# Performance work log

Measured on AMD Instinct MI355X. Metric: run time of the kernel, lower is better.

## Reference

```python
import jax, jax.numpy as jnp
import numpy as np

B, S, D, H, F = 2, 2048, 1024, 16, 4096
DH = D // H
EPS = 1e-6


def setup_inputs() -> dict:
    key = jax.random.key(0)
    ks = jax.random.split(key, 8)
    x = jax.random.normal(ks[0], (B, S, D), dtype=jnp.float32)
    # causal mask, broadcastable over [B,H,S,S]
    attention_mask = jnp.tril(jnp.ones((S, S), dtype=bool))[None, None]
    Wqkv = jax.random.normal(ks[1], (3 * D, D), dtype=jnp.float32) * (1.0 / np.sqrt(D))
    Wout = jax.random.normal(ks[2], (D, D), dtype=jnp.float32) * (1.0 / np.sqrt(D))
    W1 = jax.random.normal(ks[3], (F, D), dtype=jnp.float32) * (1.0 / np.sqrt(D))
    b1 = jnp.zeros((F,), dtype=jnp.float32)
    W2 = jax.random.normal(ks[4], (D, F), dtype=jnp.float32) * (1.0 / np.sqrt(F))
    b2 = jnp.zeros((D,), dtype=jnp.float32)
    gamma1 = jnp.ones((D,), dtype=jnp.float32)
    beta1 = jnp.zeros((D,), dtype=jnp.float32)
    gamma2 = jnp.ones((D,), dtype=jnp.float32)
    beta2 = jnp.zeros((D,), dtype=jnp.float32)
    return {"x": x, "attention_mask": attention_mask, "Wqkv": Wqkv, "Wout": Wout,
            "W1": W1, "b1": b1, "W2": W2, "b2": b2,
            "gamma1": gamma1, "beta1": beta1, "gamma2": gamma2, "beta2": beta2}


def layer_norm(x, gamma, beta):
    # Matches torch module: (x - mean) / (std + eps), std unbiased=False
    mean = jnp.mean(x, axis=-1, keepdims=True)
    std = jnp.sqrt(jnp.mean((x - mean) ** 2, axis=-1, keepdims=True))
    return gamma * ((x - mean) / (std + EPS)) + beta


def reference(x, attention_mask, Wqkv, Wout, W1, b1, W2, b2, gamma1, beta1, gamma2, beta2):
    # --- attention sub-block (Pre-LN) ---
    h = layer_norm(x, gamma1, beta1)
    qkv = h @ Wqkv.T                                   # [B,S,3D]
    qkv = qkv.reshape(B, S, 3, H, DH).transpose(2, 0, 3, 1, 4)  # [3,B,H,S,DH]
    q, k, v = qkv[0], qkv[1], qkv[2]
    scale = DH ** -0.5
    scores = jnp.einsum('bhqd,bhkd->bhqk', q, k) * scale
    scores = jnp.where(attention_mask, scores, -jnp.inf)
    attn = jax.nn.softmax(scores, axis=-1)
    out = jnp.einsum('bhqk,bhkd->bhqd', attn, v)       # [B,H,S,DH]
    out = out.transpose(0, 2, 1, 3).reshape(B, S, D)
    out = out @ Wout.T
    x = x + out                                        # dropout eval = identity
    # --- FFN sub-block (Pre-LN) ---
    h = layer_norm(x, gamma2, beta2)
    h = jax.nn.gelu(h @ W1.T + b1, approximate=False)  # torch GELU default = exact erf
    h = h @ W2.T + b2
    return x + h
```

## Files before the change

### kernel.cpp

```cpp
#include <hip/hip_runtime.h>
#include <hip/hip_bf16.h>
#include <math.h>


typedef __bf16 bf16;
typedef __bf16 bf16x4 __attribute__((ext_vector_type(4)));
typedef __bf16 bf16x8 __attribute__((ext_vector_type(8)));
typedef float f32x4 __attribute__((ext_vector_type(4)));

#define LOG2E 1.4426950408889634f
#define NSHIFT -17.312340489f

__device__ __forceinline__ f32x4 mfma16(bf16x8 a, bf16x8 b, f32x4 c) {
    return __builtin_amdgcn_mfma_f32_16x16x32_bf16(a, b, c, 0, 0, 0);
}
__device__ __forceinline__ void load16_lds(const bf16* g, bf16* l) {
    __builtin_amdgcn_global_load_lds(
        (__attribute__((address_space(1))) void*)g,
        (__attribute__((address_space(3))) void*)l, 16, 0, 0);
}

__global__ __launch_bounds__(256) void cvt4_kernel(const float* __restrict__ s0,
                                                   const float* __restrict__ s1,
                                                   const float* __restrict__ s2,
                                                   const float* __restrict__ s3,
                                                   bf16* __restrict__ dst) {
    const int blk = blockIdx.x;
    const float* s;
    int base;
    if (blk < 3072)      { s = s0; base = blk * 1024; }
    else if (blk < 4096) { s = s1; base = (blk - 3072) * 1024; }
    else if (blk < 8192) { s = s2; base = (blk - 4096) * 1024; }
    else                 { s = s3; base = (blk - 8192) * 1024; }
    const int t4 = threadIdx.x * 4;
    const float4 f = *(const float4*)(s + base + t4);
    bf16x4 o;
    o[0] = (bf16)f.x; o[1] = (bf16)f.y; o[2] = (bf16)f.z; o[3] = (bf16)f.w;
    *(bf16x4*)(dst + (size_t)blk * 1024 + t4) = o;
}

__global__ __launch_bounds__(256) void ln_kernel(const float* __restrict__ xin,
                                                 bf16* __restrict__ out,
                                                 const float* __restrict__ gamma,
                                                 const float* __restrict__ beta) {
    const int row = blockIdx.x;
    const int tid = threadIdx.x;
    const float4 f = *(const float4*)(xin + (size_t)row * 1024 + tid * 4);
    float v[4] = {f.x, f.y, f.z, f.w};
    float s = v[0] + v[1] + v[2] + v[3];
    float s2 = v[0] * v[0] + v[1] * v[1] + v[2] * v[2] + v[3] * v[3];
#pragma unroll
    for (int off = 1; off < 64; off <<= 1) {
        s += __shfl_xor(s, off);
        s2 += __shfl_xor(s2, off);
    }
    __shared__ float red[8];
    const int wave = tid >> 6, lane = tid & 63;
    if (lane == 0) { red[wave] = s; red[4 + wave] = s2; }
    __syncthreads();
    s = red[0] + red[1] + red[2] + red[3];
    s2 = red[4] + red[5] + red[6] + red[7];
    const float mean = s * (1.0f / 1024.0f);
    float var = s2 * (1.0f / 1024.0f) - mean * mean;
    var = fmaxf(var, 0.0f);
    const float rstd = 1.0f / (sqrtf(var) + 1e-6f);
    const int c = tid * 4;
    const float4 g = *(const float4*)(gamma + c);
    const float4 b = *(const float4*)(beta + c);
    bf16x4 o;
    o[0] = (bf16)((v[0] - mean) * rstd * g.x + b.x);
    o[1] = (bf16)((v[1] - mean) * rstd * g.y + b.y);
    o[2] = (bf16)((v[2] - mean) * rstd * g.z + b.z);
    o[3] = (bf16)((v[3] - mean) * rstd * g.w + b.w);
    *(bf16x4*)(out + (size_t)row * 1024 + c) = o;
}

template <int EPI>
__global__ __launch_bounds__(256, 3) void gemm_bt(const bf16* __restrict__ A,
                                                  const bf16* __restrict__ B,
                                                  int N, int K, int ldk,
                                                  bf16* __restrict__ outb,
                                                  float* __restrict__ outf,
                                                  const float* __restrict__ bias,
                                                  const float* __restrict__ resf,
                                                  bf16* __restrict__ qk,
                                                  bf16* __restrict__ vt) {
    __shared__ alignas(16) bf16 As[2][128 * 32];
    __shared__ alignas(16) bf16 Bs[2][128 * 32];
    const int tid = threadIdx.x;
    const int bm = blockIdx.x, bn = blockIdx.y;
    const int wave = tid >> 6, lane = tid & 63;
    const int wm = (wave >> 1) * 64, wn = (wave & 1) * 64;
    const int l16 = lane & 15, quad = lane >> 4;

    f32x4 acc[4][4] = {};

    const size_t koff = (size_t)blockIdx.z * K;
    const int row0 = tid >> 2, ch0 = tid & 3;
    const int gch = ch0 ^ ((row0 >> 1) & 3);
    const bf16* Ap = A + (size_t)(bm * 128 + row0) * ldk + koff + gch * 8;
    const bf16* Bp = B + (size_t)(bn * 128 + row0) * ldk + koff + gch * 8;
    const size_t rstep = (size_t)64 * ldk;

#pragma unroll
    for (int r = 0; r < 2; r++) {
        load16_lds(Ap + r * rstep, &As[0][tid * 8 + r * 2048]);
        load16_lds(Bp + r * rstep, &Bs[0][tid * 8 + r * 2048]);
    }
    __syncthreads();

    int buf = 0;
    for (int k0 = 0; k0 < K; k0 += 32, buf ^= 1) {
        if (k0 + 32 < K) {
#pragma unroll
            for (int r = 0; r < 2; r++) {
                load16_lds(Ap + r * rstep + k0 + 32, &As[buf ^ 1][tid * 8 + r * 2048]);
                load16_lds(Bp + r * rstep + k0 + 32, &Bs[buf ^ 1][tid * 8 + r * 2048]);
            }
        }
        bf16x8 af[4], bfr[4];
#pragma unroll
        for (int i = 0; i < 4; i++) {
            const int ra = wm + i * 16 + l16;
            af[i] = *(const bf16x8*)(&As[buf][ra * 32 + (quad ^ ((ra >> 1) & 3)) * 8]);
        }
#pragma unroll
        for (int j = 0; j < 4; j++) {
            const int rb = wn + j * 16 + l16;
            bfr[j] = *(const bf16x8*)(&Bs[buf][rb * 32 + (quad ^ ((rb >> 1) & 3)) * 8]);
        }
#pragma unroll
        for (int i = 0; i < 4; i++)
#pragma unroll
            for (int j = 0; j < 4; j++) acc[i][j] = mfma16(af[i], bfr[j], acc[i][j]);
        __syncthreads();
    }

#pragma unroll
    for (int i = 0; i < 4; i++) {
#pragma unroll
        for (int j = 0; j < 4; j++) {
            const int gr0 = bm * 128 + wm + i * 16 + quad * 4;
            const int gc = bn * 128 + wn + j * 16 + l16;
            float bv = 0.0f;
            if (EPI == 2) bv = bias[gc];
            if (EPI == 5 && bias && blockIdx.z == 0) bv = bias[gc];
            if (EPI == 4 && gc >= 2048) {
                const int n = gc - 2048;
                const int hh = n >> 6, dd = n & 63;
                const int bb = gr0 >> 11, ss = gr0 & 2047;
                bf16x4 pk;
#pragma unroll
                for (int r = 0; r < 4; r++) pk[r] = (bf16)acc[i][j][r];
                *(bf16x4*)(vt + ((size_t)((bb * 16 + hh) * 64 + dd)) * 2048 + ss) = pk;
            } else {
#pragma unroll
                for (int r = 0; r < 4; r++) {
                    const float v = acc[i][j][r];
                    const size_t idx = (size_t)(gr0 + r) * N + gc;
                    if (EPI == 0) {
                        outb[idx] = (bf16)v;
                    } else if (EPI == 1) {
                        outf[idx] = v + resf[idx];
                    } else if (EPI == 2) {
                        const float t = v + bv;
                        outb[idx] = (bf16)(0.5f * t * (1.0f + erff(t * 0.70710678118654752f)));
                    } else if (EPI == 5) {
                        atomicAdd(&outf[idx], v + bv);
                    } else {
                        qk[(size_t)(gr0 + r) * 2048 + gc] = (bf16)v;
                    }
                }
            }
        }
    }
}

__global__ __launch_bounds__(256, 4) void flash_attn(const bf16* __restrict__ qk,
                                                     const bf16* __restrict__ vt,
                                                     bf16* __restrict__ attn) {
    __shared__ alignas(16) bf16 Ks[64 * 72];
    __shared__ alignas(16) bf16 Vs[64 * 72];
    __shared__ alignas(16) bf16 Ps[4][16 * 72];
    const int tid = threadIdx.x;
    const int wave = tid >> 6, lane = tid & 63;
    const int l16 = lane & 15, quad = lane >> 4;
    const int bh = blockIdx.x;
    const int qt = 31 - blockIdx.y;
    const int b = bh >> 4, h = bh & 15;
    const int q0w = qt * 64 + wave * 16;
    const bf16* qkb = qk + (size_t)b * 2048 * 2048;
    const bf16* vtb = vt + (size_t)bh * 64 * 2048;

    bf16x8 qf[2];
#pragma unroll
    for (int c = 0; c < 2; c++) {
        bf16x8 v = *(const bf16x8*)(qkb + (size_t)(q0w + l16) * 2048 +
                                    h * 64 + c * 32 + quad * 8);
#pragma unroll
        for (int e = 0; e < 8; e++) v[e] = (bf16)((float)v[e] * 0.125f);
        qf[c] = v;
    }

    float lsum[4] = {0.0f, 0.0f, 0.0f, 0.0f};
    f32x4 o[4] = {};

    const int ntiles = qt + 1;
    for (int t = 0; t < ntiles; t++) {
        const int k0 = t * 64;
#pragma unroll
        for (int i = 0; i < 2; i++) {
            const int r = i * 32 + (tid >> 3), ch = tid & 7;
            *(uint4*)(&Ks[r * 72 + ch * 8]) =
                *(const uint4*)(qkb + (size_t)(k0 + r) * 2048 + 1024 + h * 64 + ch * 8);
            *(uint4*)(&Vs[r * 72 + ch * 8]) =
                *(const uint4*)(vtb + (size_t)r * 2048 + k0 + ch * 8);
        }
        __syncthreads();
        f32x4 s[4];
#pragma unroll
        for (int kt = 0; kt < 4; kt++) {
            const bf16x8 k0f = *(const bf16x8*)(&Ks[(kt * 16 + l16) * 72 + quad * 8]);
            const bf16x8 k1f = *(const bf16x8*)(&Ks[(kt * 16 + l16) * 72 + 32 + quad * 8]);
            s[kt] = mfma16(qf[1], k1f, mfma16(qf[0], k0f, (f32x4){0, 0, 0, 0}));
        }
        const bool need_mask = (t == ntiles - 1);
#pragma unroll
        for (int r = 0; r < 4; r++) {
            const int qrow = q0w + quad * 4 + r;
            float e0 = exp2f(fmaf(s[0][r], LOG2E, NSHIFT));
            float e1 = exp2f(fmaf(s[1][r], LOG2E, NSHIFT));
            float e2 = exp2f(fmaf(s[2][r], LOG2E, NSHIFT));
            float e3 = exp2f(fmaf(s[3][r], LOG2E, NSHIFT));
            if (need_mask) {
                if (k0 + l16 > qrow) e0 = 0.0f;
                if (k0 + 16 + l16 > qrow) e1 = 0.0f;
                if (k0 + 32 + l16 > qrow) e2 = 0.0f;
                if (k0 + 48 + l16 > qrow) e3 = 0.0f;
            }
            lsum[r] += (e0 + e1) + (e2 + e3);
            bf16* pp = &Ps[wave][(quad * 4 + r) * 72];
            pp[l16] = (bf16)e0;
            pp[16 + l16] = (bf16)e1;
            pp[32 + l16] = (bf16)e2;
            pp[48 + l16] = (bf16)e3;
        }
#pragma unroll
        for (int c = 0; c < 2; c++) {
            const bf16x8 pf = *(const bf16x8*)(&Ps[wave][l16 * 72 + c * 32 + quad * 8]);
#pragma unroll
            for (int dt = 0; dt < 4; dt++) {
                const bf16x8 vf =
                    *(const bf16x8*)(&Vs[(dt * 16 + l16) * 72 + c * 32 + quad * 8]);
                o[dt] = mfma16(pf, vf, o[dt]);
            }
        }
        __syncthreads();
    }

#pragma unroll
    for (int r = 0; r < 4; r++) {
#pragma unroll
        for (int off = 1; off < 16; off <<= 1) lsum[r] += __shfl_xor(lsum[r], off);
        lsum[r] = 1.0f / fmaxf(lsum[r], 1e-30f);
    }
    bf16* ob = attn + (size_t)b * 2048 * 1024;
#pragma unroll
    for (int dt = 0; dt < 4; dt++)
#pragma unroll
        for (int r = 0; r < 4; r++) {
            const int q = q0w + quad * 4 + r;
            ob[(size_t)q * 1024 + h * 64 + dt * 16 + l16] = (bf16)(o[dt][r] * lsum[r]);
        }
}

extern "C" void kernel_launch(void* const* d_in, const int* in_sizes, int n_in,
                              void* d_out, int out_size, void* d_ws, size_t ws_size,
                              hipStream_t stream) {
    const float* x    = (const float*)d_in[0];
    const float* Wqkv = (const float*)d_in[2];
    const float* Wout = (const float*)d_in[3];
    const float* W1   = (const float*)d_in[4];
    const float* b1   = (const float*)d_in[5];
    const float* W2   = (const float*)d_in[6];
    const float* b2   = (const float*)d_in[7];
    const float* g1   = (const float*)d_in[8];
    const float* be1  = (const float*)d_in[9];
    const float* g2   = (const float*)d_in[10];
    const float* be2  = (const float*)d_in[11];

    char* ws = (char*)d_ws;
    bf16* Wb     = (bf16*)(ws);
    bf16* Wqkv_b = (bf16*)(ws);
    bf16* Wout_b = (bf16*)(ws + (6u << 20));
    bf16* W1_b   = (bf16*)(ws + (8u << 20));
    bf16* W2_b   = (bf16*)(ws + (16u << 20));
    bf16* h      = (bf16*)(ws + (24u << 20));
    bf16* qkbuf  = (bf16*)(ws + (32u << 20));
    bf16* vtbuf  = (bf16*)(ws + (48u << 20));
    bf16* attn   = (bf16*)(ws + (56u << 20));
    bf16* act    = (bf16*)(ws + (32u << 20));
    float* x2    = (float*)d_out;

    cvt4_kernel<<<12288, 256, 0, stream>>>(Wqkv, Wout, W1, W2, Wb);

    ln_kernel<<<4096, 256, 0, stream>>>(x, h, g1, be1);
    gemm_bt<4><<<dim3(32, 24), 256, 0, stream>>>(h, Wqkv_b, 3072, 1024, 1024,
                                                 nullptr, nullptr, nullptr, nullptr,
                                                 qkbuf, vtbuf);
    flash_attn<<<dim3(32, 32), 256, 0, stream>>>(qkbuf, vtbuf, attn);
    gemm_bt<1><<<dim3(32, 8), 256, 0, stream>>>(attn, Wout_b, 1024, 1024, 1024,
                                                nullptr, x2, nullptr, x, nullptr, nullptr);
    ln_kernel<<<4096, 256, 0, stream>>>(x2, h, g2, be2);
    gemm_bt<2><<<dim3(32, 32), 256, 0, stream>>>(h, W1_b, 4096, 1024, 1024,
                                                 act, nullptr, b1, nullptr, nullptr, nullptr);
    gemm_bt<5><<<dim3(32, 8, 2), 256, 0, stream>>>(act, W2_b, 1024, 2048, 4096,
                                                   nullptr, x2, b2, nullptr, nullptr, nullptr);
}
```

Before: 379.9 us.

## Add 256x256x64 GEMM kernel for QKV, FFN1 and split-K FFN2

Adds a 512-thread GEMM with 256x256 output tiles and a 64-wide K step, using an 8-chunk XOR swizzle in LDS. It replaces the 128x128 kernel for the QKV projection, FFN up-projection with GELU, and FFN down-projection, which now splits K four ways instead of two. Larger tiles raise arithmetic intensity and cut global traffic per FLOP. The cost is far fewer blocks (192/256 on a 256-CU part), 128KB LDS per block limiting occupancy, and more atomic adds in the down-projection.

```diff
diff --git a/kernel.cpp b/kernel.cpp
--- a/kernel.cpp
+++ b/kernel.cpp
@@ -82,9 +82,7 @@
                                                   bf16* __restrict__ outb,
                                                   float* __restrict__ outf,
                                                   const float* __restrict__ bias,
-                                                  const float* __restrict__ resf,
-                                                  bf16* __restrict__ qk,
-                                                  bf16* __restrict__ vt) {
+                                                  const float* __restrict__ resf) {
     __shared__ alignas(16) bf16 As[2][128 * 32];
     __shared__ alignas(16) bf16 Bs[2][128 * 32];
     const int tid = threadIdx.x;
@@ -95,11 +93,10 @@
 
     f32x4 acc[4][4] = {};
 
-    const size_t koff = (size_t)blockIdx.z * K;
     const int row0 = tid >> 2, ch0 = tid & 3;
     const int gch = ch0 ^ ((row0 >> 1) & 3);
-    const bf16* Ap = A + (size_t)(bm * 128 + row0) * ldk + koff + gch * 8;
-    const bf16* Bp = B + (size_t)(bn * 128 + row0) * ldk + koff + gch * 8;
+    const bf16* Ap = A + (size_t)(bm * 128 + row0) * ldk + gch * 8;
+    const bf16* Bp = B + (size_t)(bn * 128 + row0) * ldk + gch * 8;
     const size_t rstep = (size_t)64 * ldk;
 
 #pragma unroll
@@ -142,6 +139,94 @@
         for (int j = 0; j < 4; j++) {
             const int gr0 = bm * 128 + wm + i * 16 + quad * 4;
             const int gc = bn * 128 + wn + j * 16 + l16;
+#pragma unroll
+            for (int r = 0; r < 4; r++) {
+                const float v = acc[i][j][r];
+                const size_t idx = (size_t)(gr0 + r) * N + gc;
+                if (EPI == 1) {
+                    outf[idx] = v + resf[idx];
+                } else {
+                    outb[idx] = (bf16)v;
+                }
+            }
+        }
+    }
+}
+
+template <int EPI>
+__global__ __launch_bounds__(512, 2) void gemm256_bt(const bf16* __restrict__ A,
+                                                     const bf16* __restrict__ B,
+                                                     int N, int K, int ldk,
+                                                     bf16* __restrict__ outb,
+                                                     float* __restrict__ outf,
+                                                     const float* __restrict__ bias,
+                                                     bf16* __restrict__ qk,
+                                                     bf16* __restrict__ vt) {
+    __shared__ alignas(16) bf16 As[2][256 * 64];
+    __shared__ alignas(16) bf16 Bs[2][256 * 64];
+    const int tid = threadIdx.x;
+    const int bm = blockIdx.x, bn = blockIdx.y;
+    const int wave = tid >> 6, lane = tid & 63;
+    const int wm = (wave >> 2) * 128, wn = (wave & 3) * 64;
+    const int l16 = lane & 15, quad = lane >> 4;
+
+    f32x4 acc[8][4] = {};
+
+    const size_t koff = (size_t)blockIdx.z * K;
+    const int row0 = tid >> 3, ch0 = tid & 7;
+    const int gch = ch0 ^ (row0 & 7);
+    const bf16* Ap = A + (size_t)(bm * 256 + row0) * ldk + koff + gch * 8;
+    const bf16* Bp = B + (size_t)(bn * 256 + row0) * ldk + koff + gch * 8;
+    const size_t rstep = (size_t)64 * ldk;
+
+#pragma unroll
+    for (int r = 0; r < 4; r++) {
+        load16_lds(Ap + r * rstep, &As[0][(row0 + r * 64) * 64 + ch0 * 8]);
+        load16_lds(Bp + r * rstep, &Bs[0][(row0 + r * 64) * 64 + ch0 * 8]);
+    }
+    __syncthreads();
+
+    int buf = 0;
+    for (int k0 = 0; k0 < K; k0 += 64, buf ^= 1) {
+        if (k0 + 64 < K) {
+#pragma unroll
+            for (int r = 0; r < 4; r++) {
+                load16_lds(Ap + r * rstep + k0 + 64,
+                           &As[buf ^ 1][(row0 + r * 64) * 64 + ch0 * 8]);
+                load16_lds(Bp + r * rstep + k0 + 64,
+                           &Bs[buf ^ 1][(row0 + r * 64) * 64 + ch0 * 8]);
+            }
+        }
+#pragma unroll
+        for (int kk = 0; kk < 2; kk++) {
+            bf16x8 af[8], bfr[4];
+#pragma unroll
+            for (int i = 0; i < 8; i++) {
+                const int ra = wm + i * 16 + l16;
+                af[i] = *(const bf16x8*)(
+                    &As[buf][ra * 64 + ((kk * 4 + quad) ^ (ra & 7)) * 8]);
+            }
+#pragma unroll
+            for (int j = 0; j < 4; j++) {
+                const int rb = wn + j * 16 + l16;
+                bfr[j] = *(const bf16x8*)(
+                    &Bs[buf][rb * 64 + ((kk * 4 + quad) ^ (rb & 7)) * 8]);
+            }
+#pragma unroll
+            for (int i = 0; i < 8; i++)
+#pragma unroll
+                for (int j = 0; j < 4; j++)
+                    acc[i][j] = mfma16(af[i], bfr[j], acc[i][j]);
+        }
+        __syncthreads();
+    }
+
+#pragma unroll
+    for (int i = 0; i < 8; i++) {
+#pragma unroll
+        for (int j = 0; j < 4; j++) {
+            const int gr0 = bm * 256 + wm + i * 16 + quad * 4;
+            const int gc = bn * 256 + wn + j * 16 + l16;
             float bv = 0.0f;
             if (EPI == 2) bv = bias[gc];
             if (EPI == 5 && bias && blockIdx.z == 0) bv = bias[gc];
@@ -158,11 +243,7 @@
                 for (int r = 0; r < 4; r++) {
                     const float v = acc[i][j][r];
                     const size_t idx = (size_t)(gr0 + r) * N + gc;
-                    if (EPI == 0) {
-                        outb[idx] = (bf16)v;
-                    } else if (EPI == 1) {
-                        outf[idx] = v + resf[idx];
-                    } else if (EPI == 2) {
+                    if (EPI == 2) {
                         const float t = v + bv;
                         outb[idx] = (bf16)(0.5f * t * (1.0f + erff(t * 0.70710678118654752f)));
                     } else if (EPI == 5) {
@@ -305,15 +386,15 @@
     cvt4_kernel<<<12288, 256, 0, stream>>>(Wqkv, Wout, W1, W2, Wb);
 
     ln_kernel<<<4096, 256, 0, stream>>>(x, h, g1, be1);
-    gemm_bt<4><<<dim3(32, 24), 256, 0, stream>>>(h, Wqkv_b, 3072, 1024, 1024,
-                                                 nullptr, nullptr, nullptr, nullptr,
-                                                 qkbuf, vtbuf);
+    gemm256_bt<4><<<dim3(16, 12), 512, 0, stream>>>(h, Wqkv_b, 3072, 1024, 1024,
+                                                    nullptr, nullptr, nullptr,
+                                                    qkbuf, vtbuf);
     flash_attn<<<dim3(32, 32), 256, 0, stream>>>(qkbuf, vtbuf, attn);
     gemm_bt<1><<<dim3(32, 8), 256, 0, stream>>>(attn, Wout_b, 1024, 1024, 1024,
-                                                nullptr, x2, nullptr, x, nullptr, nullptr);
+                                                nullptr, x2, nullptr, x);
     ln_kernel<<<4096, 256, 0, stream>>>(x2, h, g2, be2);
-    gemm_bt<2><<<dim3(32, 32), 256, 0, stream>>>(h, W1_b, 4096, 1024, 1024,
-                                                 act, nullptr, b1, nullptr, nullptr, nullptr);
-    gemm_bt<5><<<dim3(32, 8, 2), 256, 0, stream>>>(act, W2_b, 1024, 2048, 4096,
-                                                   nullptr, x2, b2, nullptr, nullptr, nullptr);
-}
+    gemm256_bt<2><<<dim3(16, 16), 512, 0, stream>>>(h, W1_b, 4096, 1024, 1024,
+                                                    act, nullptr, b1, nullptr, nullptr);
+    gemm256_bt<5><<<dim3(16, 4, 4), 512, 0, stream>>>(act, W2_b, 1024, 1024, 4096,
+                                                      nullptr, x2, b2, nullptr, nullptr);
+}
```

Result: slower. 470.6 us (+23.9%).

## Triple-buffer GEMM LDS loads with vmcnt-based waits and MFMA priority boost

Applied to the files above, without the earlier changes.

The bf16 GEMM main loop moves from a double-buffered LDS pipeline with a full __syncthreads per K step to a three-stage ring buffer. Two tiles are prefetched ahead, and the loop waits only on the older loads via s_waitcnt vmcnt(4) before a raw s_barrier. The MFMA block runs under raised wave priority. This is meant to hide global-load latency better and avoid draining all outstanding loads at each step, at the cost of 50% more LDS per block, which may limit occupancy at 3 blocks per CU.

```diff
diff --git a/kernel.cpp b/kernel.cpp
--- a/kernel.cpp
+++ b/kernel.cpp
@@ -75,6 +75,15 @@
     *(bf16x4*)(out + (size_t)row * 1024 + c) = o;
 }
 
+#define STAGE(tt, bi)                                              \
+    do {                                                           \
+        const int _k0 = (tt) << 5;                                 \
+        load16_lds(Ap + _k0, &As[bi][tid * 8]);                    \
+        load16_lds(Bp + _k0, &Bs[bi][tid * 8]);                    \
+        load16_lds(Ap + rstep + _k0, &As[bi][tid * 8 + 2048]);     \
+        load16_lds(Bp + rstep + _k0, &Bs[bi][tid * 8 + 2048]);     \
+    } while (0)
+
 template <int EPI>
 __global__ __launch_bounds__(256, 3) void gemm_bt(const bf16* __restrict__ A,
                                                   const bf16* __restrict__ B,
@@ -85,8 +94,8 @@
                                                   const float* __restrict__ resf,
                                                   bf16* __restrict__ qk,
                                                   bf16* __restrict__ vt) {
-    __shared__ alignas(16) bf16 As[2][128 * 32];
-    __shared__ alignas(16) bf16 Bs[2][128 * 32];
+    __shared__ alignas(16) bf16 As[3][128 * 32];
+    __shared__ alignas(16) bf16 Bs[3][128 * 32];
     const int tid = threadIdx.x;
     const int bm = blockIdx.x, bn = blockIdx.y;
     const int wave = tid >> 6, lane = tid & 63;
@@ -102,38 +111,46 @@
     const bf16* Bp = B + (size_t)(bn * 128 + row0) * ldk + koff + gch * 8;
     const size_t rstep = (size_t)64 * ldk;
 
-#pragma unroll
-    for (int r = 0; r < 2; r++) {
-        load16_lds(Ap + r * rstep, &As[0][tid * 8 + r * 2048]);
-        load16_lds(Bp + r * rstep, &Bs[0][tid * 8 + r * 2048]);
-    }
-    __syncthreads();
-
-    int buf = 0;
-    for (int k0 = 0; k0 < K; k0 += 32, buf ^= 1) {
-        if (k0 + 32 < K) {
-#pragma unroll
-            for (int r = 0; r < 2; r++) {
-                load16_lds(Ap + r * rstep + k0 + 32, &As[buf ^ 1][tid * 8 + r * 2048]);
-                load16_lds(Bp + r * rstep + k0 + 32, &Bs[buf ^ 1][tid * 8 + r * 2048]);
-            }
-        }
+    const int nt = K >> 5;
+
+    STAGE(0, 0);
+    STAGE(1, 1);
+    asm volatile("s_waitcnt vmcnt(4)" ::: "memory");
+    __builtin_amdgcn_s_barrier();
+    asm volatile("" ::: "memory");
+
+    int i0 = 0, i1 = 1, i2 = 2;
+    for (int t = 0; t < nt; ++t) {
+        if (t + 2 < nt) STAGE(t + 2, i2);
+
         bf16x8 af[4], bfr[4];
 #pragma unroll
         for (int i = 0; i < 4; i++) {
             const int ra = wm + i * 16 + l16;
-            af[i] = *(const bf16x8*)(&As[buf][ra * 32 + (quad ^ ((ra >> 1) & 3)) * 8]);
+            af[i] = *(const bf16x8*)(&As[i0][ra * 32 + (quad ^ ((ra >> 1) & 3)) * 8]);
         }
 #pragma unroll
         for (int j = 0; j < 4; j++) {
             const int rb = wn + j * 16 + l16;
-            bfr[j] = *(const bf16x8*)(&Bs[buf][rb * 32 + (quad ^ ((rb >> 1) & 3)) * 8]);
-        }
+            bfr[j] = *(const bf16x8*)(&Bs[i0][rb * 32 + (quad ^ ((rb >> 1) & 3)) * 8]);
+        }
+        __builtin_amdgcn_s_setprio(1);
 #pragma unroll
         for (int i = 0; i < 4; i++)
 #pragma unroll
             for (int j = 0; j < 4; j++) acc[i][j] = mfma16(af[i], bfr[j], acc[i][j]);
-        __syncthreads();
+        __builtin_amdgcn_s_setprio(0);
+
+        if (t + 2 < nt) {
+            asm volatile("s_waitcnt vmcnt(4)" ::: "memory");
+        } else if (t + 1 < nt) {
+            asm volatile("s_waitcnt vmcnt(0)" ::: "memory");
+        }
+        if (t + 1 < nt) {
+            __builtin_amdgcn_s_barrier();
+            asm volatile("" ::: "memory");
+        }
+        const int tmp = i0; i0 = i1; i1 = i2; i2 = tmp;
     }
 
 #pragma unroll
@@ -175,6 +192,7 @@
         }
     }
 }
+#undef STAGE
 
 __global__ __launch_bounds__(256, 4) void flash_attn(const bf16* __restrict__ qk,
                                                      const bf16* __restrict__ vt,
```

Result: slower. 392.6 us (+3.3%).
